# Performance work log

Hardware: AMD Instinct MI355X
Metric: run time of the kernel (lower is better)

## Reference

```python
import jax, jax.numpy as jnp
import numpy as np
from jax import lax

K = 3          # spline order
G = 5          # grid intervals
R0, R1 = -4.0, 4.0  # grid_range
IN, HID, OUT = 32, 128, 16
BATCH, SEQ = 256, 512


def make_grid(n_in):
    # extended knot vector: G+2K+1 knots per input, uniform spacing h
    h = (R1 - R0) / G
    knots = R0 + h * jnp.arange(-K, G + K + 1, dtype=jnp.float32)  # [G+2K+1]
    return jnp.broadcast_to(knots, (n_in, G + 2 * K + 1))


def b_splines(x, grid):
    # Cox-de Boor recursion. x: [B, n], grid: [n, G+2K+1] -> basis [B, n, G+K]
    xg = x[..., None]
    B = ((xg >= grid[:, :-1]) & (xg < grid[:, 1:])).astype(x.dtype)
    for d in range(1, K + 1):
        B = ((xg - grid[:, :-(d + 1)]) / (grid[:, d:-1] - grid[:, :-(d + 1)]) * B[..., :-1]
             + (grid[:, d + 1:] - xg) / (grid[:, d + 1:] - grid[:, 1:-d]) * B[..., 1:])
    return B


def kan_layer(x, coef, scale_base, scale_sp, grid):
    # y[b,o] = sum_i scale_base[i,o]*silu(x[b,i]) + scale_sp[i,o]*spline_io(x[b,i])
    base = jax.nn.silu(x)                               # [B, n_in]
    Bsp = b_splines(x, grid)                            # [B, n_in, G+K]
    spline = jnp.einsum('bik,iok->bio', Bsp, coef)      # [B, n_in, n_out]
    return (jnp.einsum('bi,io->bo', base, scale_base)
            + jnp.einsum('bio,io->bo', spline, scale_sp))


def setup_inputs() -> dict:
    key = jax.random.key(0)
    ks = jax.random.split(key, 7)
    x = jax.random.normal(ks[0], (BATCH, SEQ, IN), dtype=jnp.float32)
    coef1 = jax.random.normal(ks[1], (IN + HID, HID, G + K), dtype=jnp.float32) * 0.1
    sb1 = jax.random.normal(ks[2], (IN + HID, HID), dtype=jnp.float32) * 0.05
    sp1 = jax.random.normal(ks[3], (IN + HID, HID), dtype=jnp.float32) * 0.05
    coef2 = jax.random.normal(ks[4], (HID, OUT, G + K), dtype=jnp.float32) * 0.1
    sb2 = jax.random.normal(ks[5], (HID, OUT), dtype=jnp.float32) * 0.05
    sp2 = jax.random.normal(ks[6], (HID, OUT), dtype=jnp.float32) * 0.05
    return {"x": x, "coef1": coef1, "sb1": sb1, "sp1": sp1,
            "coef2": coef2, "sb2": sb2, "sp2": sp2}


def reference(x, coef1, sb1, sp1, coef2, sb2, sp2):
    grid1 = make_grid(IN + HID)
    grid2 = make_grid(HID)

    def step(h, x_t):
        combined = jnp.concatenate([x_t, h], axis=1)        # [B, IN+HID]
        h_new = kan_layer(combined, coef1, sb1, sp1, grid1)  # [B, HID]
        out_t = kan_layer(h_new, coef2, sb2, sp2, grid2)     # [B, OUT]
        return h_new, out_t

    h0 = jnp.zeros((x.shape[0], HID), dtype=x.dtype)
    _, outs = lax.scan(step, h0, jnp.swapaxes(x, 0, 1))  # outs: [T, B, OUT]
    # original stacks all timestep outputs then returns outputs[:, -1, :]
    return outs[-1]
```

## Files before the change

### kernel.cpp

```cpp
#include <hip/hip_runtime.h>
#include <hip/hip_bf16.h>

#define NIN 32
#define NHID 128
#define NOUT 16
#define NIN1 160
#define SEQT 512
#define NB 256

typedef __attribute__((ext_vector_type(8))) short s16x8;
typedef __attribute__((ext_vector_type(4))) float f32x4;

__device__ __forceinline__ unsigned int f2bfbits(float f) {
    unsigned int u = __float_as_uint(f);
    return (u + 0x7fffu + ((u >> 16) & 1u)) >> 16;
}
__device__ __forceinline__ unsigned int packbf(float lo, float hi) {
    return f2bfbits(lo) | (f2bfbits(hi) << 16);
}

__device__ __forceinline__ void spline_feat(float c, float* out4, int* jst) {
    const float t0 = -8.8f, inv_h = 0.625f;
    float u  = (c - t0) * inv_h;
    float uf = floorf(u);
    int   m0 = (int)uf;
    bool valid = (m0 >= 0) && (m0 <= 10);
    float f   = u - uf;
    float omf = 1.0f - f;
    float f2 = f * f, f3 = f2 * f;
    float omf3 = omf * omf * omf;
    const float c6 = 0.16666667f;
    float v0 = omf3 * c6;
    float v1 = __builtin_fmaf(3.0f, f3, __builtin_fmaf(-6.0f, f2, 4.0f)) * c6;
    float v2 = __builtin_fmaf(-3.0f, f3, __builtin_fmaf(3.0f, f + f2, 1.0f)) * c6;
    float v3 = f3 * c6;
    float v[4] = {v0, v1, v2, v3};
    int jb = m0 - 3;
    int js = jb < 0 ? 0 : (jb > 4 ? 4 : jb);
    int sh = js - jb;
    #pragma unroll
    for (int r = 0; r < 4; ++r) {
        int rs = r + sh;
        out4[r] = (valid && rs >= 0 && rs <= 3) ? v[rs] : 0.f;
    }
    *jst = js;
}

__device__ __forceinline__ float fsilu(float c) {
    return c * __builtin_amdgcn_rcpf(1.f + __expf(-c));
}

#define R20(X) X(0) X(1) X(2) X(3) X(4) X(5) X(6) X(7) X(8) X(9) \
               X(10) X(11) X(12) X(13) X(14) X(15) X(16) X(17) X(18) X(19)
#define R10A(X) X(0) X(1) X(2) X(3) X(4) X(5) X(6) X(7) X(8) X(9)
#define R10B(X) X(10) X(11) X(12) X(13) X(14) X(15) X(16) X(17) X(18) X(19)
#define O8(X) X(0) X(1) X(2) X(3) X(4) X(5) X(6) X(7)
#define K5(X) X(0) X(1) X(2) X(3) X(4)

__attribute__((amdgpu_waves_per_eu(2, 2)))
__global__ void __launch_bounds__(512)
kan_seq(const float* __restrict__ x,
        const float* __restrict__ coef1,
        const float* __restrict__ sb1,
        const float* __restrict__ sp1,
        const float* __restrict__ coef2,
        const float* __restrict__ sb2,
        const float* __restrict__ sp2,
        float* __restrict__ out)
{
    __shared__ __align__(16) unsigned int scr[8][20][4];
    __shared__ __align__(16) float part[2][16][NHID];
    __shared__ float Hf[NHID][9];

    const int tid  = threadIdx.x;
    const int b    = blockIdx.x;
    const int lane = tid & 63;
    const int w    = tid >> 6;
    const int arow = lane & 15;
    const int agrp = lane >> 4;
    const int rec20 = w * 20 + lane;

#define DECLW(k) uint4 wf##k##_0, wf##k##_1, wf##k##_2, wf##k##_3, \
                       wf##k##_4, wf##k##_5, wf##k##_6, wf##k##_7;
    K5(DECLW)
#undef DECLW

#define INITW1(k,t) { \
    int rec = (w * 5 + (k)) * 4 + agrp; \
    int oo  = (t) * 16 + arow; \
    const float4* cp = (const float4*)(coef1 + (size_t)(rec * NHID + oo) * 8); \
    float sp = sp1[rec * NHID + oo]; \
    float4 c0 = cp[0], c1 = cp[1]; \
    wf##k##_##t = make_uint4(packbf(sp * c0.x, sp * c0.y), packbf(sp * c0.z, sp * c0.w), \
                             packbf(sp * c1.x, sp * c1.y), packbf(sp * c1.z, sp * c1.w)); }
#define INITWK(k) INITW1(k,0) INITW1(k,1) INITW1(k,2) INITW1(k,3) \
                  INITW1(k,4) INITW1(k,5) INITW1(k,6) INITW1(k,7)
    K5(INITWK)
#undef INITWK
#undef INITW1

#define DECLSB(p) unsigned int sbp##p;
    R20(DECLSB)
#undef DECLSB
#define INITSB(p) { int i = w * 20 + (p); \
    sbp##p = packbf(sb1[i * NHID + lane], sb1[i * NHID + lane + 64]); }
    R20(INITSB)
#undef INITSB

    #pragma unroll
    for (int z = 0; z < 8; ++z) ((float*)part)[tid + 512 * z] = 0.f;
    float xv = 0.f;
    if (lane < 20 && rec20 < NIN) xv = x[(size_t)b * SEQT * NIN + rec20];
    __syncthreads();

    for (int t = 0; t < SEQT; ++t) {
        const int rb = t & 1, wb = rb ^ 1;

        float xv_use = xv;
        if (lane < 20 && rec20 < NIN) {
            int tn = (t + 1 < SEQT) ? (t + 1) : t;
            xv = x[((size_t)b * SEQT + tn) * NIN + rec20];
        }
        float silu_f = 0.f;
        if (lane < 20) {
            float c;
            if (rec20 < NIN) c = xv_use;
            else {
                int hi = rec20 - NIN;
                float s0 = (part[rb][0][hi] + part[rb][1][hi]) + (part[rb][2][hi] + part[rb][3][hi]);
                float s1 = (part[rb][4][hi] + part[rb][5][hi]) + (part[rb][6][hi] + part[rb][7][hi]);
                float s2 = (part[rb][8][hi] + part[rb][9][hi]) + (part[rb][10][hi] + part[rb][11][hi]);
                float s3 = (part[rb][12][hi] + part[rb][13][hi]) + (part[rb][14][hi] + part[rb][15][hi]);
                c = (s0 + s1) + (s2 + s3);
            }
            silu_f = fsilu(c);
            float b4[4]; int js;
            spline_feat(c, b4, &js);
            float e[8];
            #pragma unroll
            for (int k = 0; k < 8; ++k) {
                int d = k - js;
                e[k] = (d >= 0 && d < 4) ? b4[d] : 0.f;
            }
            uint4 pk;
            pk.x = packbf(e[0], e[1]); pk.y = packbf(e[2], e[3]);
            pk.z = packbf(e[4], e[5]); pk.w = packbf(e[6], e[7]);
            *(uint4*)&scr[w][lane][0] = pk;
        }

        float bc_a = 0.f, bc_b = 0.f;
#define DOTB(p) { \
        float sb_lo = __uint_as_float(sbp##p << 16); \
        float sb_hi = __uint_as_float(sbp##p & 0xffff0000u); \
        float slr = __int_as_float(__builtin_amdgcn_readlane(__float_as_int(silu_f), (p))); \
        bc_a = __builtin_fmaf(slr, sb_lo, bc_a); \
        bc_b = __builtin_fmaf(slr, sb_hi, bc_b); }
        R10A(DOTB)

        asm volatile("s_waitcnt lgkmcnt(0)" ::: "memory");
        __builtin_amdgcn_sched_barrier(0);
        uint4 bq0 = *(const uint4*)&scr[w][agrp][0];
        uint4 bq1 = *(const uint4*)&scr[w][4 + agrp][0];

        R10B(DOTB)
#undef DOTB
        part[wb][8 + w][lane] = bc_a;
        part[wb][8 + w][lane + 64] = bc_b;

        f32x4 ac0 = {0.f,0.f,0.f,0.f}, ac1 = {0.f,0.f,0.f,0.f},
              ac2 = {0.f,0.f,0.f,0.f}, ac3 = {0.f,0.f,0.f,0.f},
              ac4 = {0.f,0.f,0.f,0.f}, ac5 = {0.f,0.f,0.f,0.f},
              ac6 = {0.f,0.f,0.f,0.f}, ac7 = {0.f,0.f,0.f,0.f};
#define MMROW(k, bqv) { s16x8 bb_ = __builtin_bit_cast(s16x8, bqv); \
        ac0 = __builtin_amdgcn_mfma_f32_16x16x32_bf16(__builtin_bit_cast(s16x8, wf##k##_0), bb_, ac0, 0, 0, 0); \
        ac1 = __builtin_amdgcn_mfma_f32_16x16x32_bf16(__builtin_bit_cast(s16x8, wf##k##_1), bb_, ac1, 0, 0, 0); \
        ac2 = __builtin_amdgcn_mfma_f32_16x16x32_bf16(__builtin_bit_cast(s16x8, wf##k##_2), bb_, ac2, 0, 0, 0); \
        ac3 = __builtin_amdgcn_mfma_f32_16x16x32_bf16(__builtin_bit_cast(s16x8, wf##k##_3), bb_, ac3, 0, 0, 0); \
        ac4 = __builtin_amdgcn_mfma_f32_16x16x32_bf16(__builtin_bit_cast(s16x8, wf##k##_4), bb_, ac4, 0, 0, 0); \
        ac5 = __builtin_amdgcn_mfma_f32_16x16x32_bf16(__builtin_bit_cast(s16x8, wf##k##_5), bb_, ac5, 0, 0, 0); \
        ac6 = __builtin_amdgcn_mfma_f32_16x16x32_bf16(__builtin_bit_cast(s16x8, wf##k##_6), bb_, ac6, 0, 0, 0); \
        ac7 = __builtin_amdgcn_mfma_f32_16x16x32_bf16(__builtin_bit_cast(s16x8, wf##k##_7), bb_, ac7, 0, 0, 0); }
        MMROW(0, bq0)  uint4 bq2 = *(const uint4*)&scr[w][8 + agrp][0];
        MMROW(1, bq1)  uint4 bq3 = *(const uint4*)&scr[w][12 + agrp][0];
        MMROW(2, bq2)  uint4 bq4 = *(const uint4*)&scr[w][16 + agrp][0];
        MMROW(3, bq3)
        MMROW(4, bq4)
#undef MMROW

#define WRR(tt) if ((lane & 15) == (tt)) \
            *(f32x4*)&part[wb][w][(tt) * 16 + (agrp << 2)] = ac##tt;
        O8(WRR)
#undef WRR
        __syncthreads();
    }

    if (tid < NHID) {
        float s0 = (part[0][0][tid] + part[0][1][tid]) + (part[0][2][tid] + part[0][3][tid]);
        float s1 = (part[0][4][tid] + part[0][5][tid]) + (part[0][6][tid] + part[0][7][tid]);
        float s2 = (part[0][8][tid] + part[0][9][tid]) + (part[0][10][tid] + part[0][11][tid]);
        float s3 = (part[0][12][tid] + part[0][13][tid]) + (part[0][14][tid] + part[0][15][tid]);
        float c = (s0 + s1) + (s2 + s3);
        float sil = fsilu(c);
        float b4[4]; int js;
        spline_feat(c, b4, &js);
        #pragma unroll
        for (int k = 0; k < 8; ++k) {
            int d = k - js;
            Hf[tid][k] = (d >= 0 && d < 4) ? b4[d] : 0.f;
        }
        Hf[tid][8] = sil;
    }
    __syncthreads();
    if (tid < 128) {
        int o2 = tid & 15, isg = tid >> 4;
        float acc = 0.f;
        for (int q = 0; q < 16; ++q) {
            int i = isg * 16 + q;
            const float* c2 = coef2 + (size_t)(i * NOUT + o2) * 8;
            float s = 0.f;
            #pragma unroll
            for (int k = 0; k < 8; ++k) s += Hf[i][k] * c2[k];
            acc += Hf[i][8] * sb2[i * NOUT + o2] + sp2[i * NOUT + o2] * s;
        }
        ((float*)part)[isg * 16 + o2] = acc;
    }
    __syncthreads();
    if (tid < NOUT) {
        float a = 0.f;
        #pragma unroll
        for (int g = 0; g < 8; ++g) a += ((float*)part)[g * 16 + tid];
        out[(size_t)b * NOUT + tid] = a;
    }
}

extern "C" void kernel_launch(void* const* d_in, const int* in_sizes, int n_in,
                              void* d_out, int out_size, void* d_ws, size_t ws_size,
                              hipStream_t stream) {
    kan_seq<<<NB, 512, 0, stream>>>(
        (const float*)d_in[0], (const float*)d_in[1], (const float*)d_in[2],
        (const float*)d_in[3], (const float*)d_in[4], (const float*)d_in[5],
        (const float*)d_in[6], (float*)d_out);
}
```

Before: 1.070 ms.

## Fold SiLU base term into MFMA as sixth k-block, halve partial-sum buffer

The per-wave SiLU·scale_base dot product, previously done with 20 readlane+FMA steps per timestep, is moved into the matrix core as an extra 16x16x32 MFMA k-block. Its weights are packed as bf16 with zero padding, and the SiLU activations are written to a new shared buffer. This drops the separate base-partial rows, so the reduction over partials in the recurrence shrinks from 16 to 8. The first MFMA also uses a zero accumulator constant instead of zero-initialised registers. In exchange it adds a sixth set of weight registers, extra MFMAs and bf16 rounding of SiLU and sb1.

```diff
diff --git a/kernel.cpp b/kernel.cpp
--- a/kernel.cpp
+++ b/kernel.cpp
@@ -4,7 +4,6 @@
 #define NIN 32
 #define NHID 128
 #define NOUT 16
-#define NIN1 160
 #define SEQT 512
 #define NB 256
 
@@ -50,12 +49,15 @@
     return c * __builtin_amdgcn_rcpf(1.f + __expf(-c));
 }
 
-#define R20(X) X(0) X(1) X(2) X(3) X(4) X(5) X(6) X(7) X(8) X(9) \
-               X(10) X(11) X(12) X(13) X(14) X(15) X(16) X(17) X(18) X(19)
-#define R10A(X) X(0) X(1) X(2) X(3) X(4) X(5) X(6) X(7) X(8) X(9)
-#define R10B(X) X(10) X(11) X(12) X(13) X(14) X(15) X(16) X(17) X(18) X(19)
+__device__ __forceinline__ float sb1_pad(const float* __restrict__ sb1, int w, int k20, int oo) {
+    int kk = (k20 < 20) ? k20 : 0;
+    float v = sb1[(w * 20 + kk) * NHID + oo];
+    return (k20 < 20) ? v : 0.f;
+}
+
 #define O8(X) X(0) X(1) X(2) X(3) X(4) X(5) X(6) X(7)
 #define K5(X) X(0) X(1) X(2) X(3) X(4)
+#define K6(X) X(0) X(1) X(2) X(3) X(4) X(5)
 
 __attribute__((amdgpu_waves_per_eu(2, 2)))
 __global__ void __launch_bounds__(512)
@@ -69,7 +71,8 @@
         float* __restrict__ out)
 {
     __shared__ __align__(16) unsigned int scr[8][20][4];
-    __shared__ __align__(16) float part[2][16][NHID];
+    __shared__ __align__(16) unsigned short scrS[8][32];
+    __shared__ __align__(16) float part[2][8][NHID];
     __shared__ float Hf[NHID][9];
 
     const int tid  = threadIdx.x;
@@ -82,7 +85,7 @@
 
 #define DECLW(k) uint4 wf##k##_0, wf##k##_1, wf##k##_2, wf##k##_3, \
                        wf##k##_4, wf##k##_5, wf##k##_6, wf##k##_7;
-    K5(DECLW)
+    K6(DECLW)
 #undef DECLW
 
 #define INITW1(k,t) { \
@@ -99,18 +102,23 @@
 #undef INITWK
 #undef INITW1
 
-#define DECLSB(p) unsigned int sbp##p;
-    R20(DECLSB)
-#undef DECLSB
-#define INITSB(p) { int i = w * 20 + (p); \
-    sbp##p = packbf(sb1[i * NHID + lane], sb1[i * NHID + lane + 64]); }
-    R20(INITSB)
-#undef INITSB
+#define INITW5(t) { \
+    int oo = (t) * 16 + arow; \
+    int kb = agrp * 8; \
+    float e0 = sb1_pad(sb1, w, kb + 0, oo), e1 = sb1_pad(sb1, w, kb + 1, oo); \
+    float e2 = sb1_pad(sb1, w, kb + 2, oo), e3 = sb1_pad(sb1, w, kb + 3, oo); \
+    float e4 = sb1_pad(sb1, w, kb + 4, oo), e5 = sb1_pad(sb1, w, kb + 5, oo); \
+    float e6 = sb1_pad(sb1, w, kb + 6, oo), e7 = sb1_pad(sb1, w, kb + 7, oo); \
+    wf5_##t = make_uint4(packbf(e0, e1), packbf(e2, e3), packbf(e4, e5), packbf(e6, e7)); }
+    O8(INITW5)
+#undef INITW5
 
     #pragma unroll
-    for (int z = 0; z < 8; ++z) ((float*)part)[tid + 512 * z] = 0.f;
+    for (int z = 0; z < 4; ++z) ((float*)part)[tid + 512 * z] = 0.f;
+    if (tid < 128) ((unsigned int*)scrS)[tid] = 0u;
     float xv = 0.f;
     if (lane < 20 && rec20 < NIN) xv = x[(size_t)b * SEQT * NIN + rec20];
+    const f32x4 zq = {0.f, 0.f, 0.f, 0.f};
     __syncthreads();
 
     for (int t = 0; t < SEQT; ++t) {
@@ -121,7 +129,6 @@
             int tn = (t + 1 < SEQT) ? (t + 1) : t;
             xv = x[((size_t)b * SEQT + tn) * NIN + rec20];
         }
-        float silu_f = 0.f;
         if (lane < 20) {
             float c;
             if (rec20 < NIN) c = xv_use;
@@ -129,11 +136,9 @@
                 int hi = rec20 - NIN;
                 float s0 = (part[rb][0][hi] + part[rb][1][hi]) + (part[rb][2][hi] + part[rb][3][hi]);
                 float s1 = (part[rb][4][hi] + part[rb][5][hi]) + (part[rb][6][hi] + part[rb][7][hi]);
-                float s2 = (part[rb][8][hi] + part[rb][9][hi]) + (part[rb][10][hi] + part[rb][11][hi]);
-                float s3 = (part[rb][12][hi] + part[rb][13][hi]) + (part[rb][14][hi] + part[rb][15][hi]);
-                c = (s0 + s1) + (s2 + s3);
+                c = s0 + s1;
             }
-            silu_f = fsilu(c);
+            float sil = fsilu(c);
             float b4[4]; int js;
             spline_feat(c, b4, &js);
             float e[8];
@@ -146,31 +151,24 @@
             pk.x = packbf(e[0], e[1]); pk.y = packbf(e[2], e[3]);
             pk.z = packbf(e[4], e[5]); pk.w = packbf(e[6], e[7]);
             *(uint4*)&scr[w][lane][0] = pk;
-        }
-
-        float bc_a = 0.f, bc_b = 0.f;
-#define DOTB(p) { \
-        float sb_lo = __uint_as_float(sbp##p << 16); \
-        float sb_hi = __uint_as_float(sbp##p & 0xffff0000u); \
-        float slr = __int_as_float(__builtin_amdgcn_readlane(__float_as_int(silu_f), (p))); \
-        bc_a = __builtin_fmaf(slr, sb_lo, bc_a); \
-        bc_b = __builtin_fmaf(slr, sb_hi, bc_b); }
-        R10A(DOTB)
+            scrS[w][lane] = (unsigned short)f2bfbits(sil);
+        }
 
         asm volatile("s_waitcnt lgkmcnt(0)" ::: "memory");
         __builtin_amdgcn_sched_barrier(0);
         uint4 bq0 = *(const uint4*)&scr[w][agrp][0];
         uint4 bq1 = *(const uint4*)&scr[w][4 + agrp][0];
 
-        R10B(DOTB)
-#undef DOTB
-        part[wb][8 + w][lane] = bc_a;
-        part[wb][8 + w][lane + 64] = bc_b;
-
-        f32x4 ac0 = {0.f,0.f,0.f,0.f}, ac1 = {0.f,0.f,0.f,0.f},
-              ac2 = {0.f,0.f,0.f,0.f}, ac3 = {0.f,0.f,0.f,0.f},
-              ac4 = {0.f,0.f,0.f,0.f}, ac5 = {0.f,0.f,0.f,0.f},
-              ac6 = {0.f,0.f,0.f,0.f}, ac7 = {0.f,0.f,0.f,0.f};
+        f32x4 ac0, ac1, ac2, ac3, ac4, ac5, ac6, ac7;
+#define MMROW0(k, bqv) { s16x8 bb_ = __builtin_bit_cast(s16x8, bqv); \
+        ac0 = __builtin_amdgcn_mfma_f32_16x16x32_bf16(__builtin_bit_cast(s16x8, wf##k##_0), bb_, zq, 0, 0, 0); \
+        ac1 = __builtin_amdgcn_mfma_f32_16x16x32_bf16(__builtin_bit_cast(s16x8, wf##k##_1), bb_, zq, 0, 0, 0); \
+        ac2 = __builtin_amdgcn_mfma_f32_16x16x32_bf16(__builtin_bit_cast(s16x8, wf##k##_2), bb_, zq, 0, 0, 0); \
+        ac3 = __builtin_amdgcn_mfma_f32_16x16x32_bf16(__builtin_bit_cast(s16x8, wf##k##_3), bb_, zq, 0, 0, 0); \
+        ac4 = __builtin_amdgcn_mfma_f32_16x16x32_bf16(__builtin_bit_cast(s16x8, wf##k##_4), bb_, zq, 0, 0, 0); \
+        ac5 = __builtin_amdgcn_mfma_f32_16x16x32_bf16(__builtin_bit_cast(s16x8, wf##k##_5), bb_, zq, 0, 0, 0); \
+        ac6 = __builtin_amdgcn_mfma_f32_16x16x32_bf16(__builtin_bit_cast(s16x8, wf##k##_6), bb_, zq, 0, 0, 0); \
+        ac7 = __builtin_amdgcn_mfma_f32_16x16x32_bf16(__builtin_bit_cast(s16x8, wf##k##_7), bb_, zq, 0, 0, 0); }
 #define MMROW(k, bqv) { s16x8 bb_ = __builtin_bit_cast(s16x8, bqv); \
         ac0 = __builtin_amdgcn_mfma_f32_16x16x32_bf16(__builtin_bit_cast(s16x8, wf##k##_0), bb_, ac0, 0, 0, 0); \
         ac1 = __builtin_amdgcn_mfma_f32_16x16x32_bf16(__builtin_bit_cast(s16x8, wf##k##_1), bb_, ac1, 0, 0, 0); \
@@ -180,14 +178,16 @@
         ac5 = __builtin_amdgcn_mfma_f32_16x16x32_bf16(__builtin_bit_cast(s16x8, wf##k##_5), bb_, ac5, 0, 0, 0); \
         ac6 = __builtin_amdgcn_mfma_f32_16x16x32_bf16(__builtin_bit_cast(s16x8, wf##k##_6), bb_, ac6, 0, 0, 0); \
         ac7 = __builtin_amdgcn_mfma_f32_16x16x32_bf16(__builtin_bit_cast(s16x8, wf##k##_7), bb_, ac7, 0, 0, 0); }
-        MMROW(0, bq0)  uint4 bq2 = *(const uint4*)&scr[w][8 + agrp][0];
-        MMROW(1, bq1)  uint4 bq3 = *(const uint4*)&scr[w][12 + agrp][0];
-        MMROW(2, bq2)  uint4 bq4 = *(const uint4*)&scr[w][16 + agrp][0];
-        MMROW(3, bq3)
+        MMROW0(0, bq0)  uint4 bq2 = *(const uint4*)&scr[w][8 + agrp][0];
+        MMROW(1, bq1)   uint4 bq3 = *(const uint4*)&scr[w][12 + agrp][0];
+        MMROW(2, bq2)   uint4 bq4 = *(const uint4*)&scr[w][16 + agrp][0];
+        MMROW(3, bq3)   uint4 bq5 = *(const uint4*)&scrS[w][agrp * 8];
         MMROW(4, bq4)
+        MMROW(5, bq5)
 #undef MMROW
-
-#define WRR(tt) if ((lane & 15) == (tt)) \
+#undef MMROW0
+
+#define WRR(tt) if (arow == (tt)) \
             *(f32x4*)&part[wb][w][(tt) * 16 + (agrp << 2)] = ac##tt;
         O8(WRR)
 #undef WRR
@@ -197,9 +197,7 @@
     if (tid < NHID) {
         float s0 = (part[0][0][tid] + part[0][1][tid]) + (part[0][2][tid] + part[0][3][tid]);
         float s1 = (part[0][4][tid] + part[0][5][tid]) + (part[0][6][tid] + part[0][7][tid]);
-        float s2 = (part[0][8][tid] + part[0][9][tid]) + (part[0][10][tid] + part[0][11][tid]);
-        float s3 = (part[0][12][tid] + part[0][13][tid]) + (part[0][14][tid] + part[0][15][tid]);
-        float c = (s0 + s1) + (s2 + s3);
+        float c = s0 + s1;
         float sil = fsilu(c);
         float b4[4]; int js;
         spline_feat(c, b4, &js);
```

New measurement: 979.0 us. -8.5%, faster.
